# Kernel optimization log

Hardware: AMD Instinct MI355X
Metric: run time of the kernel (lower is better)

The kernel has to match this reference:

```python
import jax, jax.numpy as jnp
import numpy as np
from jax.ops import segment_sum, segment_max

DIM = 64; EDGE_DIM = 6; ACTION_DIM = 6
N = 16384; E = 32768; G = 256; TPG = 12  # nodes, edges, graphs, torsions/graph


def setup_inputs() -> dict:
    key = jax.random.key(0)
    ks = jax.random.split(key, 16)
    d = DIM
    def lin(k, fo, fi):
        return (jax.random.normal(k, (fo, fi), jnp.float32) / np.sqrt(fi)).astype(jnp.float32)
    return {
        "x": jax.random.normal(ks[0], (N, 3), jnp.float32),
        "edge_attr": jax.random.normal(ks[1], (E, EDGE_DIM), jnp.float32),
        "edge_index": jax.random.randint(ks[2], (2, E), 0, N),
        "batch": (jnp.arange(N) // (N // G)).astype(jnp.int32),
        "nonring": jax.random.randint(ks[3], (G * TPG, 4), 0, N),
        "nrbidx": (jnp.arange(G * TPG) // TPG).astype(jnp.int32),
        "num_graphs": G,
        "torsion_size": TPG,
        "lin0_w": lin(ks[4], d, 3), "lin0_b": jnp.zeros((d,), jnp.float32),
        "e1_w": lin(ks[5], d, EDGE_DIM), "e1_b": jnp.zeros((d,), jnp.float32),
        "e2_w": lin(ks[6], d * d, d), "e2_b": jnp.zeros((d * d,), jnp.float32),
        "root_w": lin(ks[7], d, d), "conv_b": jnp.zeros((d,), jnp.float32),
        "gru_wih": lin(ks[8], 3 * d, d), "gru_whh": lin(ks[9], 3 * d, d),
        "gru_bih": jnp.zeros((3 * d,), jnp.float32), "gru_bhh": jnp.zeros((3 * d,), jnp.float32),
        "s2s_wih": lin(ks[10], 4 * d, 2 * d), "s2s_whh": lin(ks[11], 4 * d, d),
        "s2s_bih": jnp.zeros((4 * d,), jnp.float32), "s2s_bhh": jnp.zeros((4 * d,), jnp.float32),
        "mem_wih": lin(ks[12], 4 * d, 2 * d), "mem_whh": lin(ks[13], 4 * d, d),
        "mem_bih": jnp.zeros((4 * d,), jnp.float32), "mem_bhh": jnp.zeros((4 * d,), jnp.float32),
        "lin1_w": lin(ks[14], d, 5 * d), "lin1_b": jnp.zeros((d,), jnp.float32),
        "lin2_w": lin(ks[15], ACTION_DIM, d), "lin2_b": jnp.zeros((ACTION_DIM,), jnp.float32),
    }


def _lstm_step(xin, h, c, wih, whh, bih, bhh):
    g = xin @ wih.T + bih + h @ whh.T + bhh
    i, f, gg, o = jnp.split(g, 4, axis=-1)
    c = jax.nn.sigmoid(f) * c + jax.nn.sigmoid(i) * jnp.tanh(gg)
    h = jax.nn.sigmoid(o) * jnp.tanh(c)
    return h, c


def _model(x, edge_attr, lin0_w, lin0_b, e1_w, e1_b, e2_w, e2_b, root_w, conv_b,
           gru_wih, gru_whh, gru_bih, gru_bhh, s2s_wih, s2s_whh, s2s_bih, s2s_bhh,
           mem_wih, mem_whh, mem_bih, mem_bhh, lin1_w, lin1_b, lin2_w, lin2_b,
           edge_index, batch, nonring, nrbidx, num_graphs, torsion_size):
    d = lin0_w.shape[0]
    n = x.shape[0]
    out = jax.nn.relu(x @ lin0_w.T + lin0_b)           # [N, d]
    h = out                                            # GRU hidden
    src, dst = edge_index[0], edge_index[1]
    # edge-conditioned weights (fixed across the 6 iterations -> computed once)
    ew = (jax.nn.relu(edge_attr @ e1_w.T + e1_b) @ e2_w.T + e2_b).reshape(-1, d, d)  # [E, d, d]
    deg = jnp.clip(segment_sum(jnp.ones((src.shape[0],), out.dtype), dst, num_segments=n), 1.0)
    for _ in range(6):
        msg = jnp.einsum('ei,eio->eo', out[src], ew)   # per-edge matmul, [E, d]
        agg = segment_sum(msg, dst, num_segments=n) / deg[:, None]  # scatter-mean
        m = jax.nn.relu(agg + out @ root_w + conv_b)
        gi = m @ gru_wih.T + gru_bih
        gh = h @ gru_whh.T + gru_bhh
        r = jax.nn.sigmoid(gi[:, :d] + gh[:, :d])
        z = jax.nn.sigmoid(gi[:, d:2 * d] + gh[:, d:2 * d])
        nnew = jnp.tanh(gi[:, 2 * d:] + r * gh[:, 2 * d:])
        h = (1.0 - z) * nnew + z * h
        out = h
    # Set2Set pooling, 6 processing steps
    q_star = jnp.zeros((num_graphs, 2 * d), out.dtype)
    hs = jnp.zeros((num_graphs, d), out.dtype); cs = jnp.zeros_like(hs)
    for _ in range(6):
        hs, cs = _lstm_step(q_star, hs, cs, s2s_wih, s2s_whh, s2s_bih, s2s_bhh)
        e = jnp.sum(out * hs[batch], axis=-1)
        emax = segment_max(e, batch, num_segments=num_graphs)
        a = jnp.exp(e - emax[batch])
        a = a / segment_sum(a, batch, num_segments=num_graphs)[batch]
        r_ = segment_sum(a[:, None] * out, batch, num_segments=num_graphs)
        q_star = jnp.concatenate([hs, r_], axis=-1)
    # memory LSTM, single step from zero state
    hx = jnp.zeros((num_graphs, d), out.dtype); cx = jnp.zeros_like(hx)
    hx, cx = _lstm_step(q_star, hx, cx, mem_wih, mem_whh, mem_bih, mem_bhh)
    lstm_sel = hx[nrbidx]                                   # [T, d]
    node_sel = out[nonring.reshape(-1)].reshape(4, -1, d)   # faithful to .view(4,-1,dim)
    stacked = jnp.concatenate([lstm_sel[None], node_sel], axis=0)  # [5, T, d]
    feat = jnp.transpose(stacked, (2, 1, 0)).reshape(-1, 5 * d)    # faithful permute+reshape -> [T, 5d]
    o1 = jax.nn.relu(feat @ lin1_w.T + lin1_b)
    logits = o1 @ lin2_w.T + lin2_b                          # [T, action_dim]
    logit = logits.reshape(num_graphs, torsion_size, -1)     # uniform split + pad_sequence
    return logit, hx[None], cx[None]


def reference(x, edge_attr, edge_index, batch, nonring, nrbidx, num_graphs, torsion_size,
              lin0_w, lin0_b, e1_w, e1_b, e2_w, e2_b, root_w, conv_b,
              gru_wih, gru_whh, gru_bih, gru_bhh, s2s_wih, s2s_whh, s2s_bih, s2s_bhh,
              mem_wih, mem_whh, mem_bih, mem_bhh, lin1_w, lin1_b, lin2_w, lin2_b):
    return _model(x, edge_attr, lin0_w, lin0_b, e1_w, e1_b, e2_w, e2_b, root_w, conv_b,
                  gru_wih, gru_whh, gru_bih, gru_bhh, s2s_wih, s2s_whh, s2s_bih, s2s_bhh,
                  mem_wih, mem_whh, mem_bih, mem_bhh, lin1_w, lin1_b, lin2_w, lin2_b,
                  edge_index, batch, nonring, nrbidx, num_graphs, torsion_size)
```

## Files before the change

kernel.cpp:

```cpp
#include <hip/hip_runtime.h>

#define NNODE 16384
#define NEDGE 32768
#define NG    256
#define TPGx  12
#define TTOT  (NG * TPGx)
#define D     64

typedef _Float16 h8 __attribute__((ext_vector_type(8)));
typedef float    f4 __attribute__((ext_vector_type(4)));

static __device__ __forceinline__ float sigm(float x) { return 1.f / (1.f + __expf(-x)); }

static __device__ __forceinline__ f4 mfma16h(h8 a, h8 b, f4 c) {
  return __builtin_amdgcn_mfma_f32_16x16x32_f16(a, b, c, 0, 0, 0);
}

static __device__ __forceinline__ h8 splat16(_Float16 x) {
  h8 v = {x, x, x, x, x, x, x, x};
  return v;
}

static __device__ __forceinline__ void gload_lds16(const void* g, void* l) {
  __builtin_amdgcn_global_load_lds(
      (const __attribute__((address_space(1))) unsigned int*)g,
      (__attribute__((address_space(3))) unsigned int*)l, 16, 0, 0);
}

#define WS_H      0
#define WS_AGG    4194304
#define WS_W2     8388608
#define WS_RT     8921088
#define WS_WHH    8929280
#define WS_WIH    8953856
#define WS_SWIHT  8978432
#define WS_SWHHT  9109504
#define WS_MWIHT  9175040
#define WS_L1WT   9306112
#define WS_L2WF   9388032
#define WS_FB     9389568
#define WS_DEG    9398784
#define WS_HX     9464320
#define WS_NEED   9529856

struct Srcs { const void* p[23]; };

__device__ __constant__ const int kCum[24] = {
    0, 192, 256, 640, 704, 262848, 266944, 271040, 271104, 283392, 295680,
    295872, 296064, 328832, 345216, 345472, 345728, 378496, 378752, 379008,
    399488, 399552, 399936, 399942};

__global__ __launch_bounds__(256) void pack_kernel(Srcs S, char* __restrict__ ws) {
  int idx = blockIdx.x * 256 + threadIdx.x;
  if (idx >= 399942) return;
  int r = 0, base = 0;
#pragma unroll
  for (int k = 0; k < 23; k++)
    if (idx >= kCum[k]) { r = k; base = kCum[k]; }
  int li = idx - base;
  float v = ((const float*)S.p[r])[li];

  float*    fb    = (float*)(ws + WS_FB);
  _Float16* w2    = (_Float16*)(ws + WS_W2);
  _Float16* rtH   = (_Float16*)(ws + WS_RT);
  _Float16* whhH  = (_Float16*)(ws + WS_WHH);
  _Float16* wihH  = (_Float16*)(ws + WS_WIH);
  float*    swihT = (float*)(ws + WS_SWIHT);
  float*    swhhT = (float*)(ws + WS_SWHHT);
  float*    mwihT = (float*)(ws + WS_MWIHT);
  float*    l1wT  = (float*)(ws + WS_L1WT);
  float*    l2w   = (float*)(ws + WS_L2WF);

  switch (r) {
    case 0: fb[li] = v; break;
    case 1: fb[192 + li] = v; break;
    case 2: fb[256 + li] = v; break;
    case 3: fb[640 + li] = v; break;
    case 4: {
      int i = li >> 12, o = (li >> 6) & 63, k = li & 63;
      w2[i * 4096 + (((k >> 3) * 64 + o) << 3) + (k & 7)] = (_Float16)v;
    } break;
    case 5: {
      int k = li >> 6, o = li & 63;
      w2[64 * 4096 + (((k >> 3) * 64 + o) << 3) + (k & 7)] = (_Float16)v;
    } break;
    case 6: {
      int i = li >> 6, o = li & 63;
      rtH[o * 64 + i] = (_Float16)v;
    } break;
    case 7: fb[704 + li] = v; break;
    case 8: wihH[li] = (_Float16)v; break;
    case 9: whhH[li] = (_Float16)v; break;
    case 10: fb[768 + li] = v; break;
    case 11: fb[960 + li] = v; break;
    case 12: swihT[(li & 127) * 256 + (li >> 7)] = v; break;
    case 13: swhhT[(li & 63) * 256 + (li >> 6)] = v; break;
    case 14: fb[1152 + li] = v; break;
    case 15: fb[1408 + li] = v; break;
    case 16: mwihT[(li & 127) * 256 + (li >> 7)] = v; break;
    case 17: fb[1664 + li] = v; break;
    case 18: fb[1920 + li] = v; break;
    case 19: l1wT[(li % 320) * 64 + (li / 320)] = v; break;
    case 20: fb[2176 + li] = v; break;
    case 21: l2w[li] = v; break;
    case 22: fb[2240 + li] = v; break;
  }
}

__global__ __launch_bounds__(256) void init_kernel(
    const float* __restrict__ x, const float* __restrict__ fb,
    float* __restrict__ h) {
  int idx = blockIdx.x * 256 + threadIdx.x;
  int n = idx >> 6, o = idx & 63;
  float acc = fb[192 + o];
#pragma unroll
  for (int j = 0; j < 3; j++) acc += x[n * 3 + j] * fb[o * 3 + j];
  h[idx] = fmaxf(acc, 0.f);
}

__global__ __launch_bounds__(256) void deg_kernel(const int* __restrict__ edge_index,
                                                  float* __restrict__ deg) {
  int e = blockIdx.x * 256 + threadIdx.x;
  if (e < NEDGE) atomicAdd(&deg[edge_index[NEDGE + e]], 1.0f);
}

__global__ __launch_bounds__(256) void msg_kernel(
    const float* __restrict__ h, const float* __restrict__ ea,
    const float* __restrict__ fb, const _Float16* __restrict__ w2,
    const int* __restrict__ edge_index, float* __restrict__ agg) {
  __shared__ _Float16 sOut[128][72];
  __shared__ _Float16 sB[2][8192];
  const int tid = threadIdx.x;
  const int wave = tid >> 6, lane = tid & 63;
  const int m15 = lane & 15, quad = lane >> 4;
  const int eb = blockIdx.x * 128;
  {
    int r = tid >> 1, c0 = (tid & 1) * 32;
    int srcn = edge_index[eb + r];
#pragma unroll
    for (int c = c0; c < c0 + 32; c += 4) {
      float4 v = *(const float4*)&h[srcn * D + c];
      sOut[r][c]     = (_Float16)v.x;
      sOut[r][c + 1] = (_Float16)v.y;
      sOut[r][c + 2] = (_Float16)v.z;
      sOut[r][c + 3] = (_Float16)v.w;
    }
  }
  const int erow1 = wave * 16 + m15;
  const int erow2 = 64 + erow1;
  const int e1 = eb + erow1, e2 = eb + erow2;
  h8 hidA0, hidA1, hidB0, hidB1;
  {
    float eav1[6], eav2[6];
#pragma unroll
    for (int j = 0; j < 6; j++) { eav1[j] = ea[e1 * 6 + j]; eav2[j] = ea[e2 * 6 + j]; }
#pragma unroll
    for (int j = 0; j < 8; j++) {
      int k0 = quad * 8 + j, k1 = 32 + quad * 8 + j;
      float a01 = fb[640 + k0], a11 = fb[640 + k1];
      float a02 = a01, a12 = a11;
#pragma unroll
      for (int jj = 0; jj < 6; jj++) {
        float w0 = fb[256 + k0 * 6 + jj], w1 = fb[256 + k1 * 6 + jj];
        a01 += eav1[jj] * w0; a11 += eav1[jj] * w1;
        a02 += eav2[jj] * w0; a12 += eav2[jj] * w1;
      }
      hidA0[j] = (_Float16)fmaxf(a01, 0.f);
      hidA1[j] = (_Float16)fmaxf(a11, 0.f);
      hidB0[j] = (_Float16)fmaxf(a02, 0.f);
      hidB1[j] = (_Float16)fmaxf(a12, 0.f);
    }
  }
  for (int c = wave; c < 16; c += 4)
    gload_lds16(w2 + c * 512 + lane * 8, &sB[0][c * 512]);
  __syncthreads();
  f4 zz = {0.f, 0.f, 0.f, 0.f};
  f4 accA[4], accB[4];
#pragma unroll
  for (int nt = 0; nt < 4; nt++) { accA[nt] = zz; accB[nt] = zz; }
  for (int p = 0; p < 33; p++) {
    const int cur = p & 1;
    if (p < 32) {
      int nch = (p == 31) ? 8 : 16;
      const _Float16* src = w2 + (p + 1) * 8192;
      for (int c = wave; c < nch; c += 4)
        gload_lds16(src + c * 512 + lane * 8, &sB[cur ^ 1][c * 512]);
    }
    const int cnt = (p == 32) ? 1 : 2;
    for (int t = 0; t < cnt; t++) {
      const int i = p * 2 + t;
      h8 a10, a11, a20, a21;
      if (i < 64) {
        h8 o1 = splat16(sOut[erow1][i]);
        h8 o2 = splat16(sOut[erow2][i]);
        a10 = hidA0 * o1; a11 = hidA1 * o1;
        a20 = hidB0 * o2; a21 = hidB1 * o2;
      } else {
        a10 = *(const h8*)&sOut[erow1][quad * 8];
        a11 = *(const h8*)&sOut[erow1][32 + quad * 8];
        a20 = *(const h8*)&sOut[erow2][quad * 8];
        a21 = *(const h8*)&sOut[erow2][32 + quad * 8];
      }
      const _Float16* base = &sB[cur][t * 4096];
      const int q512 = quad * 512;
#pragma unroll
      for (int nt = 0; nt < 4; nt++) {
        int br8 = (nt * 16 + m15) * 8;
        h8 bh0 = *(const h8*)(base + q512 + br8);
        h8 bh1 = *(const h8*)(base + 2048 + q512 + br8);
        accA[nt] = mfma16h(a10, bh0, accA[nt]);
        accA[nt] = mfma16h(a11, bh1, accA[nt]);
        accB[nt] = mfma16h(a20, bh0, accB[nt]);
        accB[nt] = mfma16h(a21, bh1, accB[nt]);
      }
    }
    __syncthreads();
  }
#pragma unroll
  for (int reg = 0; reg < 4; reg++) {
    int r1 = eb + wave * 16 + quad * 4 + reg;
    int r2 = r1 + 64;
    int dn1 = edge_index[NEDGE + r1];
    int dn2 = edge_index[NEDGE + r2];
    float* ap1 = agg + dn1 * D;
    float* ap2 = agg + dn2 * D;
#pragma unroll
    for (int nt = 0; nt < 4; nt++) {
      atomicAdd(ap1 + nt * 16 + m15, accA[nt][reg]);
      atomicAdd(ap2 + nt * 16 + m15, accB[nt][reg]);
    }
  }
}

__global__ __launch_bounds__(256) void update_kernel(
    float* __restrict__ h, float* __restrict__ agg, const float* __restrict__ deg,
    const _Float16* __restrict__ rtH, const _Float16* __restrict__ whhH,
    const _Float16* __restrict__ wihH, const float* __restrict__ fb) {
  __shared__ float buf[64][68];
  const int tid = threadIdx.x;
  const int wave = tid >> 6, lane = tid & 63;
  const int m15 = lane & 15, quad = lane >> 4;
  const int nb = blockIdx.x * 64;
  {
    int r = tid >> 2, c0 = (tid & 3) * 16;
#pragma unroll
    for (int c = c0; c < c0 + 16; c += 4)
      *(float4*)&buf[r][c] = *(const float4*)&h[(nb + r) * D + c];
  }
  __syncthreads();
  const int mrow = wave * 16 + m15;
  h8 a0, a1;
#pragma unroll
  for (int j = 0; j < 8; j++) {
    a0[j] = (_Float16)buf[mrow][quad * 8 + j];
    a1[j] = (_Float16)buf[mrow][32 + quad * 8 + j];
  }
  f4 zz = {0.f, 0.f, 0.f, 0.f};
  f4 acc[16];
#pragma unroll
  for (int nt = 0; nt < 16; nt++) acc[nt] = zz;
#pragma unroll
  for (int nt = 0; nt < 16; nt++) {
    int nn = nt * 16 + m15;
    const _Float16* bp = (nt < 4) ? (rtH + nn * D) : (whhH + (nn - 64) * D);
    h8 bh0 = *(const h8*)(bp + quad * 8);
    h8 bh1 = *(const h8*)(bp + 32 + quad * 8);
    f4 a = acc[nt];
    a = mfma16h(a0, bh0, a);
    a = mfma16h(a1, bh1, a);
    acc[nt] = a;
  }
  __syncthreads();
#pragma unroll
  for (int nt = 0; nt < 4; nt++) {
#pragma unroll
    for (int reg = 0; reg < 4; reg++) {
      int nloc = wave * 16 + quad * 4 + reg;
      int o = nt * 16 + m15;
      float dg = fmaxf(deg[nb + nloc], 1.f);
      int aidx = (nb + nloc) * D + o;
      float v = acc[nt][reg] + agg[aidx] / dg + fb[704 + o];
      agg[aidx] = 0.f;
      buf[nloc][o] = fmaxf(v, 0.f);
    }
  }
  __syncthreads();
  h8 m0, m1;
#pragma unroll
  for (int j = 0; j < 8; j++) {
    m0[j] = (_Float16)buf[mrow][quad * 8 + j];
    m1[j] = (_Float16)buf[mrow][32 + quad * 8 + j];
  }
  f4 g2[12];
#pragma unroll
  for (int nt = 0; nt < 12; nt++) g2[nt] = zz;
#pragma unroll
  for (int nt = 0; nt < 12; nt++) {
    int nn = nt * 16 + m15;
    const _Float16* bp = wihH + nn * D;
    h8 bh0 = *(const h8*)(bp + quad * 8);
    h8 bh1 = *(const h8*)(bp + 32 + quad * 8);
    f4 a = g2[nt];
    a = mfma16h(m0, bh0, a);
    a = mfma16h(m1, bh1, a);
    g2[nt] = a;
  }
#pragma unroll
  for (int nt = 0; nt < 4; nt++) {
#pragma unroll
    for (int reg = 0; reg < 4; reg++) {
      int nloc = wave * 16 + quad * 4 + reg;
      int o = nt * 16 + m15;
      int gidx = (nb + nloc) * D + o;
      float gir = g2[nt][reg]      + fb[768 + o];
      float giz = g2[nt + 4][reg]  + fb[768 + 64 + o];
      float gin = g2[nt + 8][reg]  + fb[768 + 128 + o];
      float ghr = acc[nt + 4][reg]  + fb[960 + o];
      float ghz = acc[nt + 8][reg]  + fb[960 + 64 + o];
      float ghn = acc[nt + 12][reg] + fb[960 + 128 + o];
      float rr = sigm(gir + ghr);
      float zg = sigm(giz + ghz);
      float nnv = tanhf(gin + rr * ghn);
      float hv = h[gidx];
      h[gidx] = (1.f - zg) * nnv + zg * hv;
    }
  }
}

__global__ __launch_bounds__(256) void s2s_kernel(
    const float* __restrict__ h,
    const float* __restrict__ wihT, const float* __restrict__ whhT,
    const float* __restrict__ mwihT, const float* __restrict__ fb,
    float* __restrict__ hx_f32, float* __restrict__ dout) {
  __shared__ float outL[64][65];
  __shared__ float qs[128];
  __shared__ float hsv[64], csv[64], sg[256], sa[64];
  __shared__ float spart[4][64];
  const int t = threadIdx.x;
  const int g = blockIdx.x;
  for (int idx = t; idx < 64 * 64; idx += 256) outL[idx >> 6][idx & 63] = h[g * 4096 + idx];
  if (t < 128) qs[t] = 0.f;
  if (t < 64) { hsv[t] = 0.f; csv[t] = 0.f; }
  __syncthreads();
  for (int step = 0; step < 6; step++) {
    float acc = fb[1152 + t] + fb[1408 + t];
#pragma unroll 8
    for (int j = 0; j < 128; j++) acc += qs[j] * wihT[j * 256 + t];
#pragma unroll 8
    for (int j = 0; j < 64; j++) acc += hsv[j] * whhT[j * 256 + t];
    sg[t] = acc;
    __syncthreads();
    if (t < 64) {
      float cn = sigm(sg[64 + t]) * csv[t] + sigm(sg[t]) * tanhf(sg[128 + t]);
      csv[t] = cn;
      hsv[t] = sigm(sg[192 + t]) * tanhf(cn);
    }
    __syncthreads();
    if (t < 64) {
      float e = 0.f;
      for (int d2 = 0; d2 < 64; d2++) e += outL[t][d2] * hsv[d2];
      float mx = e;
      for (int off = 32; off > 0; off >>= 1) mx = fmaxf(mx, __shfl_xor(mx, off));
      float a = __expf(e - mx);
      float s = a;
      for (int off = 32; off > 0; off >>= 1) s += __shfl_xor(s, off);
      sa[t] = a / s;
    }
    __syncthreads();
    {
      int o = t & 63, part = t >> 6;
      float r = 0.f;
      for (int n2 = part * 16; n2 < part * 16 + 16; n2++) r += sa[n2] * outL[n2][o];
      spart[part][o] = r;
    }
    __syncthreads();
    if (t < 64) {
      qs[t] = hsv[t];
      qs[64 + t] = spart[0][t] + spart[1][t] + spart[2][t] + spart[3][t];
    }
    __syncthreads();
  }
  float acc = fb[1664 + t] + fb[1920 + t];
#pragma unroll 8
  for (int j = 0; j < 128; j++) acc += qs[j] * mwihT[j * 256 + t];
  sg[t] = acc;
  __syncthreads();
  if (t < 64) {
    float cn = sigm(sg[t]) * tanhf(sg[128 + t]);
    float hn = sigm(sg[192 + t]) * tanhf(cn);
    hx_f32[g * 64 + t] = hn;
    dout[TTOT * 6 + g * 64 + t] = hn;
    dout[TTOT * 6 + NG * 64 + g * 64 + t] = cn;
  }
}

__global__ __launch_bounds__(64) void head_kernel(
    const float* __restrict__ h, const float* __restrict__ hx_f32,
    const int* __restrict__ nonring, const int* __restrict__ nrbidx,
    const float* __restrict__ l1wT, const float* __restrict__ l2w,
    const float* __restrict__ fb, float* __restrict__ dout) {
  __shared__ float feat[320];
  __shared__ float so1[64];
  const int r = blockIdx.x;
  const int lane = threadIdx.x;
  const int blk = r % 48, di = r / 48;
  const int tt = blk * 64 + lane;
  feat[lane * 5] = hx_f32[nrbidx[tt] * 64 + di];
#pragma unroll
  for (int s = 1; s <= 4; s++)
    feat[lane * 5 + s] = h[nonring[(s - 1) * TTOT + tt] * 64 + di];
  __syncthreads();
  float acc = fb[2176 + lane];
#pragma unroll 8
  for (int c = 0; c < 320; c++) acc += feat[c] * l1wT[c * 64 + lane];
  so1[lane] = fmaxf(acc, 0.f);
  __syncthreads();
  if (lane < 6) {
    float a2 = fb[2240 + lane];
    for (int j = 0; j < 64; j++) a2 += so1[j] * l2w[lane * 64 + j];
    dout[r * 6 + lane] = a2;
  }
}

extern "C" void kernel_launch(void* const* d_in, const int* in_sizes, int n_in,
                              void* d_out, int out_size, void* d_ws, size_t ws_size,
                              hipStream_t stream) {
  (void)in_sizes; (void)n_in; (void)out_size;
  const float* x         = (const float*)d_in[0];
  const float* edge_attr = (const float*)d_in[1];
  const int* edge_index  = (const int*)d_in[2];
  const int* nonring     = (const int*)d_in[4];
  const int* nrbidx      = (const int*)d_in[5];
  float* out = (float*)d_out;

  char* ws = (char*)d_ws;
  float*    h      = (float*)(ws + WS_H);
  float*    agg    = (float*)(ws + WS_AGG);
  _Float16* w2     = (_Float16*)(ws + WS_W2);
  _Float16* rtH    = (_Float16*)(ws + WS_RT);
  _Float16* whhH   = (_Float16*)(ws + WS_WHH);
  _Float16* wihH   = (_Float16*)(ws + WS_WIH);
  float*    swihT  = (float*)(ws + WS_SWIHT);
  float*    swhhT  = (float*)(ws + WS_SWHHT);
  float*    mwihT  = (float*)(ws + WS_MWIHT);
  float*    l1wT   = (float*)(ws + WS_L1WT);
  float*    l2wF   = (float*)(ws + WS_L2WF);
  float*    fb     = (float*)(ws + WS_FB);
  float*    deg    = (float*)(ws + WS_DEG);
  float*    hx_f32 = (float*)(ws + WS_HX);
  if (ws_size < (size_t)WS_NEED) return;

  Srcs S;
  S.p[0] = d_in[8];   S.p[1] = d_in[9];   S.p[2] = d_in[10];  S.p[3] = d_in[11];
  S.p[4] = d_in[12];  S.p[5] = d_in[13];  S.p[6] = d_in[14];  S.p[7] = d_in[15];
  S.p[8] = d_in[16];  S.p[9] = d_in[17];  S.p[10] = d_in[18]; S.p[11] = d_in[19];
  S.p[12] = d_in[20]; S.p[13] = d_in[21]; S.p[14] = d_in[22]; S.p[15] = d_in[23];
  S.p[16] = d_in[24]; S.p[17] = d_in[26]; S.p[18] = d_in[27]; S.p[19] = d_in[28];
  S.p[20] = d_in[29]; S.p[21] = d_in[30]; S.p[22] = d_in[31];
  pack_kernel<<<(399942 + 255) / 256, 256, 0, stream>>>(S, ws);

  init_kernel<<<NNODE * D / 256, 256, 0, stream>>>(x, fb, h);
  hipMemsetAsync(deg, 0, NNODE * 4, stream);
  hipMemsetAsync(agg, 0, NNODE * D * 4, stream);
  deg_kernel<<<NEDGE / 256, 256, 0, stream>>>(edge_index, deg);

  for (int it = 0; it < 6; it++) {
    msg_kernel<<<NEDGE / 128, 256, 0, stream>>>(h, edge_attr, fb, w2, edge_index, agg);
    update_kernel<<<NNODE / 64, 256, 0, stream>>>(h, agg, deg, rtH, whhH, wihH, fb);
  }

  s2s_kernel<<<NG, 256, 0, stream>>>(h, swihT, swhhT, mwihT, fb, hx_f32, out);
  head_kernel<<<TTOT, 64, 0, stream>>>(h, hx_f32, nonring, nrbidx, l1wT, l2wF, fb, out);
}
```

Before: 530.3 us.

## Retile message kernel to 64 edges per block with split output columns

```diff
diff --git a/kernel.cpp b/kernel.cpp
--- a/kernel.cpp
+++ b/kernel.cpp
@@ -128,17 +128,19 @@
     const float* __restrict__ h, const float* __restrict__ ea,
     const float* __restrict__ fb, const _Float16* __restrict__ w2,
     const int* __restrict__ edge_index, float* __restrict__ agg) {
-  __shared__ _Float16 sOut[128][72];
-  __shared__ _Float16 sB[2][8192];
+  __shared__ _Float16 sOut[64][72];
+  __shared__ _Float16 sB[2][16384];
   const int tid = threadIdx.x;
   const int wave = tid >> 6, lane = tid & 63;
   const int m15 = lane & 15, quad = lane >> 4;
-  const int eb = blockIdx.x * 128;
+  const int eg = wave >> 1;
+  const int cg = wave & 1;
+  const int eb = blockIdx.x * 64;
   {
-    int r = tid >> 1, c0 = (tid & 1) * 32;
+    int r = tid >> 2, c0 = (tid & 3) * 16;
     int srcn = edge_index[eb + r];
 #pragma unroll
-    for (int c = c0; c < c0 + 32; c += 4) {
+    for (int c = c0; c < c0 + 16; c += 4) {
       float4 v = *(const float4*)&h[srcn * D + c];
       sOut[r][c]     = (_Float16)v.x;
       sOut[r][c + 1] = (_Float16)v.y;
@@ -146,9 +148,9 @@
       sOut[r][c + 3] = (_Float16)v.w;
     }
   }
-  const int erow1 = wave * 16 + m15;
-  const int erow2 = 64 + erow1;
-  const int e1 = eb + erow1, e2 = eb + erow2;
+  const int erowA = eg * 32 + m15;
+  const int erowB = erowA + 16;
+  const int e1 = eb + erowA, e2 = eb + erowB;
   h8 hidA0, hidA1, hidB0, hidB1;
   {
     float eav1[6], eav2[6];
@@ -171,63 +173,63 @@
       hidB1[j] = (_Float16)fmaxf(a12, 0.f);
     }
   }
-  for (int c = wave; c < 16; c += 4)
+  for (int c = wave; c < 32; c += 4)
     gload_lds16(w2 + c * 512 + lane * 8, &sB[0][c * 512]);
   __syncthreads();
   f4 zz = {0.f, 0.f, 0.f, 0.f};
-  f4 accA[4], accB[4];
-#pragma unroll
-  for (int nt = 0; nt < 4; nt++) { accA[nt] = zz; accB[nt] = zz; }
-  for (int p = 0; p < 33; p++) {
+  f4 accA[2], accB[2];
+#pragma unroll
+  for (int j = 0; j < 2; j++) { accA[j] = zz; accB[j] = zz; }
+  for (int p = 0; p < 17; p++) {
     const int cur = p & 1;
-    if (p < 32) {
-      int nch = (p == 31) ? 8 : 16;
-      const _Float16* src = w2 + (p + 1) * 8192;
+    if (p < 16) {
+      int nch = (p == 15) ? 8 : 32;
+      const _Float16* src = w2 + (p + 1) * 16384;
       for (int c = wave; c < nch; c += 4)
         gload_lds16(src + c * 512 + lane * 8, &sB[cur ^ 1][c * 512]);
     }
-    const int cnt = (p == 32) ? 1 : 2;
+    const int cnt = (p == 16) ? 1 : 4;
     for (int t = 0; t < cnt; t++) {
-      const int i = p * 2 + t;
+      const int i = p * 4 + t;
       h8 a10, a11, a20, a21;
       if (i < 64) {
-        h8 o1 = splat16(sOut[erow1][i]);
-        h8 o2 = splat16(sOut[erow2][i]);
+        h8 o1 = splat16(sOut[erowA][i]);
+        h8 o2 = splat16(sOut[erowB][i]);
         a10 = hidA0 * o1; a11 = hidA1 * o1;
         a20 = hidB0 * o2; a21 = hidB1 * o2;
       } else {
-        a10 = *(const h8*)&sOut[erow1][quad * 8];
-        a11 = *(const h8*)&sOut[erow1][32 + quad * 8];
-        a20 = *(const h8*)&sOut[erow2][quad * 8];
-        a21 = *(const h8*)&sOut[erow2][32 + quad * 8];
+        a10 = *(const h8*)&sOut[erowA][quad * 8];
+        a11 = *(const h8*)&sOut[erowA][32 + quad * 8];
+        a20 = *(const h8*)&sOut[erowB][quad * 8];
+        a21 = *(const h8*)&sOut[erowB][32 + quad * 8];
       }
       const _Float16* base = &sB[cur][t * 4096];
       const int q512 = quad * 512;
 #pragma unroll
-      for (int nt = 0; nt < 4; nt++) {
+      for (int j = 0; j < 2; j++) {
+        int nt = cg * 2 + j;
         int br8 = (nt * 16 + m15) * 8;
         h8 bh0 = *(const h8*)(base + q512 + br8);
         h8 bh1 = *(const h8*)(base + 2048 + q512 + br8);
-        accA[nt] = mfma16h(a10, bh0, accA[nt]);
-        accA[nt] = mfma16h(a11, bh1, accA[nt]);
-        accB[nt] = mfma16h(a20, bh0, accB[nt]);
-        accB[nt] = mfma16h(a21, bh1, accB[nt]);
+        accA[j] = mfma16h(a10, bh0, accA[j]);
+        accA[j] = mfma16h(a11, bh1, accA[j]);
+        accB[j] = mfma16h(a20, bh0, accB[j]);
+        accB[j] = mfma16h(a21, bh1, accB[j]);
       }
     }
     __syncthreads();
   }
 #pragma unroll
   for (int reg = 0; reg < 4; reg++) {
-    int r1 = eb + wave * 16 + quad * 4 + reg;
-    int r2 = r1 + 64;
-    int dn1 = edge_index[NEDGE + r1];
-    int dn2 = edge_index[NEDGE + r2];
-    float* ap1 = agg + dn1 * D;
-    float* ap2 = agg + dn2 * D;
-#pragma unroll
-    for (int nt = 0; nt < 4; nt++) {
-      atomicAdd(ap1 + nt * 16 + m15, accA[nt][reg]);
-      atomicAdd(ap2 + nt * 16 + m15, accB[nt][reg]);
+    int rA = eb + eg * 32 + quad * 4 + reg;
+    int rB = rA + 16;
+    int dnA = edge_index[NEDGE + rA];
+    int dnB = edge_index[NEDGE + rB];
+#pragma unroll
+    for (int j = 0; j < 2; j++) {
+      int o = (cg * 2 + j) * 16 + m15;
+      atomicAdd(agg + dnA * D + o, accA[j][reg]);
+      atomicAdd(agg + dnB * D + o, accB[j][reg]);
     }
   }
 }
@@ -465,7 +467,7 @@
   deg_kernel<<<NEDGE / 256, 256, 0, stream>>>(edge_index, deg);
 
   for (int it = 0; it < 6; it++) {
-    msg_kernel<<<NEDGE / 128, 256, 0, stream>>>(h, edge_attr, fb, w2, edge_index, agg);
+    msg_kernel<<<NEDGE / 64, 256, 0, stream>>>(h, edge_attr, fb, w2, edge_index, agg);
     update_kernel<<<NNODE / 64, 256, 0, stream>>>(h, agg, deg, rtH, whhH, wihH, fb);
   }
 
```

New measurement: 498.6 us. 6.0% less time.
